# Kernel optimization log

Hardware: AMD Instinct MI355X
Metric: run time of the kernel (lower is better)

## Reference

```python
import jax, jax.numpy as jnp
import numpy as np

TEMPERATURE = 11.313708498984761  # sqrt(d_k) with d_k=128
RELU15_CAP = 15.0


def setup_inputs() -> dict:
    key = jax.random.key(0)
    kq, kk, kv = jax.random.split(key, 3)
    B, H, S, D = 4, 16, 1024, 128
    q = jax.random.normal(kq, (B, H, S, D), dtype=jnp.float32)
    k = jax.random.normal(kk, (B, H, S, D), dtype=jnp.float32)
    v = jax.random.normal(kv, (B, H, S, D), dtype=jnp.float32)
    mask = jnp.ones((B, 1, S, S), dtype=jnp.int32)  # broadcast over heads
    return {"q": q, "k": k, "v": v, "mask": mask}


def reference(q, k, v, mask):
    # attn = (q / temperature) @ k^T  -> [B,H,Sq,Sk]
    attn = jnp.einsum("bhqd,bhkd->bhqk", q / TEMPERATURE, k)
    # masked_fill(mask == 0, -1e9)
    attn = jnp.where(mask == 0, jnp.float32(-1e9), attn)
    # ReLU15 activation (custom softmax replacement): clamp to [0, 15]
    attn = jnp.clip(attn, 0.0, RELU15_CAP)
    # dropout with p=0.0 is identity (inference reference)
    out = jnp.einsum("bhqk,bhkd->bhqd", attn, v)
    return (out, attn)
```

## Files before the change

kernel.cpp:

```cpp
#include <hip/hip_runtime.h>
#include <stdint.h>

#define B_   4
#define H_   16
#define S_   1024
#define D_   128
#define BM   64
#define BN   32
#define NKT  (S_ / BN)
#define NTHREADS 256

typedef float f32x4 __attribute__((ext_vector_type(4)));
typedef short s16x8 __attribute__((ext_vector_type(8)));
typedef short s16x4 __attribute__((ext_vector_type(4)));

static __device__ __forceinline__ uint16_t f2bf(float f) {
  uint32_t u = __float_as_uint(f);
  u += 0x7FFFu + ((u >> 16) & 1u);
  return (uint16_t)(u >> 16);
}
static __device__ __forceinline__ float bf2f(uint16_t h) {
  return __uint_as_float((uint32_t)h << 16);
}

#define LDS_BARRIER() do {                                   \
    asm volatile("s_waitcnt lgkmcnt(0)" ::: "memory");       \
    __builtin_amdgcn_s_barrier();                            \
    __builtin_amdgcn_sched_barrier(0);                       \
  } while (0)


__global__ __launch_bounds__(NTHREADS)
__attribute__((amdgpu_waves_per_eu(4, 4)))
void attn_relu15_kernel(const float* __restrict__ q, const float* __restrict__ k,
                        const float* __restrict__ v, const int* __restrict__ mask,
                        float* __restrict__ outp, float* __restrict__ attnp)
{
  const int blk = blockIdx.x;
  const int g   = (blk & 7) * 128 + (blk >> 3);
  const int bh  = g >> 4;
  const int qt  = g & 15;
  const int b   = bh >> 4;

  const int tid  = threadIdx.x;
  const int lane = tid & 63;
  const int wq   = tid >> 6;
  const int lhi  = lane >> 4;
  const int llo  = lane & 15;

  __shared__ __align__(16) char smem[36864];
  char* const lK0 = smem;
  char* const lV0 = smem + 16384;
  char* const lS  = smem + 32768 + wq * 1024;

  const float* qg = q + (size_t)bh * (S_ * D_) + (size_t)qt * BM * D_;
  const float* kg = k + (size_t)bh * (S_ * D_);
  const float* vg = v + (size_t)bh * (S_ * D_);
  const int*   mg = mask  + (size_t)b * S_ * S_ + (size_t)qt * BM * S_;
  float*       ag = attnp + (size_t)bh * S_ * S_ + (size_t)qt * BM * S_;
  float*       og = outp  + (size_t)bh * (S_ * D_) + (size_t)qt * BM * D_;

  const float invT = 0.08838834764831843f;

  #define K_O(rep)   ((tid + NTHREADS * (rep)) * 8)
  #define K_ROW(o)   ((((o) >> 10) & 1) * 16 + (((o) >> 4) & 15))
  #define K_COL(o)   (((o) >> 11) * 32 + (((o) >> 8) & 3) * 8 + (((o) >> 3) & 1) * 4)

  s16x8 qf[4];
  {
    const float* qrow = qg + (size_t)(16 * wq + llo) * D_;
    #pragma unroll
    for (int ks = 0; ks < 4; ++ks) {
      int d0 = 32 * ks + 8 * lhi;
      f32x4 x0 = *(const f32x4*)(qrow + d0);
      f32x4 x1 = *(const f32x4*)(qrow + d0 + 4);
      s16x8 h;
      h[0]=f2bf(x0[0]*invT); h[1]=f2bf(x0[1]*invT); h[2]=f2bf(x0[2]*invT); h[3]=f2bf(x0[3]*invT);
      h[4]=f2bf(x1[0]*invT); h[5]=f2bf(x1[1]*invT); h[6]=f2bf(x1[2]*invT); h[7]=f2bf(x1[3]*invT);
      qf[ks] = h;
    }
  }

  {
    #pragma unroll
    for (int rep = 0; rep < 4; ++rep) {
      int o = K_O(rep);
      f32x4 x = *(const f32x4*)(kg + K_ROW(o) * D_ + K_COL(o));
      s16x4 h; h[0]=f2bf(x[0]); h[1]=f2bf(x[1]); h[2]=f2bf(x[2]); h[3]=f2bf(x[3]);
      *(s16x4*)(lK0 + o) = h;
    }
    #pragma unroll
    for (int rep = 0; rep < 4; ++rep) {
      int bid = (tid >> 2) + 64 * rep;
      int kb = bid >> 5, db = bid & 31, l2 = lane & 3;
      f32x4 x = *(const f32x4*)(vg + (size_t)(kb * 4 + l2) * D_ + db * 4);
      float v0=x[0], v1=x[1], v2=x[2], v3=x[3], t;
      t=(l2&1)?v0:v1; t=__shfl_xor(t,1); if(l2&1)v0=t; else v1=t;
      t=(l2&1)?v2:v3; t=__shfl_xor(t,1); if(l2&1)v2=t; else v3=t;
      t=(l2&2)?v0:v2; t=__shfl_xor(t,2); if(l2&2)v0=t; else v2=t;
      t=(l2&2)?v1:v3; t=__shfl_xor(t,2); if(l2&2)v1=t; else v3=t;
      int dd = db * 4 + l2;
      s16x4 h; h[0]=f2bf(v0); h[1]=f2bf(v1); h[2]=f2bf(v2); h[3]=f2bf(v3);
      *(s16x4*)(lV0 + (dd >> 4) * 1024 + ((kb >> 1) & 3) * 256
                    + (dd & 15) * 16 + (kb & 1) * 8) = h;
    }
  }
  LDS_BARRIER();

  f32x4 oacc[8];
  #pragma unroll
  for (int i = 0; i < 8; ++i) oacc[i] = (f32x4){0.f,0.f,0.f,0.f};

  int cur = 0;
  for (int kt = 0; kt < NKT; ++kt) {
    const bool pf = (kt + 1 < NKT);
    char* lKc = lK0 + cur * 8192;
    char* lVc = lV0 + cur * 8192;

    f32x4 kst[4];
    const float* kgt = kg + (size_t)(kt + 1) * BN * D_;
    if (pf) {
      #pragma unroll
      for (int rep = 0; rep < 4; ++rep) {
        int o = K_O(rep);
        kst[rep] = *(const f32x4*)(kgt + K_ROW(o) * D_ + K_COL(o));
      }
    }
    int mreg[8];
    #pragma unroll
    for (int nt = 0; nt < 2; ++nt)
      #pragma unroll
      for (int j = 0; j < 4; ++j)
        mreg[nt * 4 + j] =
          mg[(size_t)(16 * wq + 4 * lhi + j) * S_ + kt * BN + 16 * nt + llo];

    f32x4 sacc[2];
    sacc[0] = (f32x4){0.f,0.f,0.f,0.f}; sacc[1] = sacc[0];
    #pragma unroll
    for (int ks = 0; ks < 4; ++ks) {
      s16x8 bfr[2];
      #pragma unroll
      for (int nt = 0; nt < 2; ++nt)
        bfr[nt] = *(s16x8*)(lKc + (ks * 2 + nt) * 1024 + lane * 16);
      #pragma unroll
      for (int nt = 0; nt < 2; ++nt)
        sacc[nt] = __builtin_amdgcn_mfma_f32_16x16x32_bf16(qf[ks], bfr[nt], sacc[nt], 0, 0, 0);
    }

    f32x4 vst[4];
    const float* vgt = vg + (size_t)(kt + 1) * BN * D_;
    if (pf) {
      char* lKn = lK0 + (cur ^ 1) * 8192;
      #pragma unroll
      for (int rep = 0; rep < 4; ++rep) {
        f32x4 x = kst[rep];
        s16x4 h; h[0]=f2bf(x[0]); h[1]=f2bf(x[1]); h[2]=f2bf(x[2]); h[3]=f2bf(x[3]);
        *(s16x4*)(lKn + K_O(rep)) = h;
      }
      #pragma unroll
      for (int rep = 0; rep < 4; ++rep) {
        int bid = (tid >> 2) + 64 * rep;
        int kb = bid >> 5, db = bid & 31, l2 = lane & 3;
        vst[rep] = *(const f32x4*)(vgt + (size_t)(kb * 4 + l2) * D_ + db * 4);
      }
    }

    #pragma unroll
    for (int nt = 0; nt < 2; ++nt) {
      char* sb = lS + (2 * nt + (llo >> 3)) * 256 + (llo & 7) * 2;
      #pragma unroll
      for (int j = 0; j < 4; ++j) {
        float val = fminf(fmaxf(sacc[nt][j], 0.f), 15.f);
        if (mreg[nt * 4 + j] == 0) val = 0.f;
        *(uint16_t*)(sb + (4 * lhi + j) * 16) = f2bf(val);
      }
    }

    {
      s16x8 saf = *(s16x8*)(lS + lane * 16);
      #pragma unroll
      for (int nt = 0; nt < 8; ++nt) {
        s16x8 vb = *(s16x8*)(lVc + nt * 1024 + lane * 16);
        oacc[nt] = __builtin_amdgcn_mfma_f32_16x16x32_bf16(saf, vb, oacc[nt], 0, 0, 0);
      }
    }

    #pragma unroll
    for (int p = 0; p < 2; ++p) {
      int r  = 16 * wq + p * 8 + (lane >> 3);
      int cb = lane & 7;
      s16x4 sv = *(s16x4*)(lS + (cb >> 1) * 256 + ((r & 15) * 16) + (cb & 1) * 8);
      f32x4 a;
      a[0]=bf2f((uint16_t)sv[0]); a[1]=bf2f((uint16_t)sv[1]);
      a[2]=bf2f((uint16_t)sv[2]); a[3]=bf2f((uint16_t)sv[3]);
      __builtin_nontemporal_store(a, (f32x4*)(ag + (size_t)r * S_ + kt * BN + cb * 4));
    }

    if (pf) {
      char* lVn = lV0 + (cur ^ 1) * 8192;
      #pragma unroll
      for (int rep = 0; rep < 4; ++rep) {
        int bid = (tid >> 2) + 64 * rep;
        int kb = bid >> 5, db = bid & 31, l2 = lane & 3;
        f32x4 x = vst[rep];
        float v0=x[0], v1=x[1], v2=x[2], v3=x[3], t;
        t=(l2&1)?v0:v1; t=__shfl_xor(t,1); if(l2&1)v0=t; else v1=t;
        t=(l2&1)?v2:v3; t=__shfl_xor(t,1); if(l2&1)v2=t; else v3=t;
        t=(l2&2)?v0:v2; t=__shfl_xor(t,2); if(l2&2)v0=t; else v2=t;
        t=(l2&2)?v1:v3; t=__shfl_xor(t,2); if(l2&2)v1=t; else v3=t;
        int dd = db * 4 + l2;
        s16x4 h; h[0]=f2bf(v0); h[1]=f2bf(v1); h[2]=f2bf(v2); h[3]=f2bf(v3);
        *(s16x4*)(lVn + (dd >> 4) * 1024 + ((kb >> 1) & 3) * 256
                      + (dd & 15) * 16 + (kb & 1) * 8) = h;
      }
    }

    LDS_BARRIER();
    cur ^= 1;
  }

  #pragma unroll
  for (int nt = 0; nt < 8; ++nt) {
    int n = 16 * nt + llo;
    #pragma unroll
    for (int j = 0; j < 4; ++j) {
      int m = 16 * wq + 4 * lhi + j;
      __builtin_nontemporal_store(oacc[nt][j], og + (size_t)m * D_ + n);
    }
  }
}

extern "C" void kernel_launch(void* const* d_in, const int* in_sizes, int n_in,
                              void* d_out, int out_size, void* d_ws, size_t ws_size,
                              hipStream_t stream) {
  const float* q    = (const float*)d_in[0];
  const float* k    = (const float*)d_in[1];
  const float* v    = (const float*)d_in[2];
  const int*   mask = (const int*)d_in[3];
  float* outp  = (float*)d_out;
  float* attnp = outp + (size_t)B_ * H_ * S_ * D_;
  dim3 grid(B_ * H_ * (S_ / BM));
  attn_relu15_kernel<<<grid, NTHREADS, 0, stream>>>(q, k, v, mask, outp, attnp);
}
```

Baseline: 125.9 us.

## Pre-convert K/V to bf16 MFMA layout and bitpack mask in a prepass kernel

Adds a prepass kernel that converts K and V to bf16 in the exact LDS fragment layout and packs the int32 mask into bitmasks in workspace. The main kernel then streams K/V tiles straight into LDS with global_load_lds and reads one mask bit per element instead of int32 loads. This removes the repeated per-query-tile fp32 conversion, the shuffle-based transpose and the 4-byte mask reads, at the cost of an extra launch and extra workspace traffic. The original kernel is kept as a fallback when the workspace is too small.

Result: faster. 101.5 us (-19.4%).

```diff
diff --git a/kernel.cpp b/kernel.cpp
--- a/kernel.cpp
+++ b/kernel.cpp
@@ -23,18 +23,63 @@
   return __uint_as_float((uint32_t)h << 16);
 }
 
-#define LDS_BARRIER() do {                                   \
-    asm volatile("s_waitcnt lgkmcnt(0)" ::: "memory");       \
-    __builtin_amdgcn_s_barrier();                            \
-    __builtin_amdgcn_sched_barrier(0);                       \
-  } while (0)
-
+static __device__ __forceinline__ void gl16(const void* g, void* l) {
+  __builtin_amdgcn_global_load_lds(
+      (const __attribute__((address_space(1))) unsigned int*)g,
+      (__attribute__((address_space(3))) unsigned int*)l, 16, 0, 0);
+}
+
+#define WSK_BYTES  16777216
+#define WSV_BYTES  16777216
+#define WSM_BYTES  524288
+#define WS_NEED    (WSK_BYTES + WSV_BYTES + WSM_BYTES)
+
+__global__ __launch_bounds__(256)
+void prepass_kernel(const float* __restrict__ k, const float* __restrict__ v,
+                    const int* __restrict__ mask,
+                    char* __restrict__ wsK, char* __restrict__ wsV,
+                    uint32_t* __restrict__ wsM)
+{
+  int gid = blockIdx.x * 256 + threadIdx.x;
+  if (gid < 1048576) {
+    int tile = gid >> 9, c = gid & 511;
+    int ks = c >> 7, nt = (c >> 6) & 1, lane = c & 63;
+    int row = (tile & 31) * 32 + 16 * nt + (lane & 15);
+    int col = 32 * ks + 8 * (lane >> 4);
+    const float* src = k + ((size_t)(tile >> 5) * S_ + row) * D_ + col;
+    f32x4 x0 = *(const f32x4*)src;
+    f32x4 x1 = *(const f32x4*)(src + 4);
+    s16x8 h;
+    h[0]=f2bf(x0[0]); h[1]=f2bf(x0[1]); h[2]=f2bf(x0[2]); h[3]=f2bf(x0[3]);
+    h[4]=f2bf(x1[0]); h[5]=f2bf(x1[1]); h[6]=f2bf(x1[2]); h[7]=f2bf(x1[3]);
+    *(s16x8*)(wsK + (size_t)gid * 16) = h;
+  } else if (gid < 2097152) {
+    int gv = gid - 1048576;
+    int tile = gv >> 9, c = gv & 511;
+    int nt = c >> 6, lane = c & 63;
+    int d   = 16 * nt + (lane & 15);
+    int kv0 = (tile & 31) * 32 + 8 * (lane >> 4);
+    const float* src = v + ((size_t)(tile >> 5) * S_ + kv0) * D_ + d;
+    s16x8 h;
+    #pragma unroll
+    for (int i = 0; i < 8; ++i) h[i] = f2bf(src[(size_t)i * D_]);
+    *(s16x8*)(wsV + (size_t)gv * 16) = h;
+  } else if (gid < 2228224) {
+    int gm = gid - 2097152;
+    const int* src = mask + (size_t)(gm >> 5) * S_ + (gm & 31) * 32;
+    uint32_t bits = 0;
+    #pragma unroll
+    for (int i = 0; i < 32; ++i) bits |= (src[i] != 0 ? 1u : 0u) << i;
+    wsM[gm] = bits;
+  }
+}
 
 __global__ __launch_bounds__(NTHREADS)
 __attribute__((amdgpu_waves_per_eu(4, 4)))
-void attn_relu15_kernel(const float* __restrict__ q, const float* __restrict__ k,
-                        const float* __restrict__ v, const int* __restrict__ mask,
-                        float* __restrict__ outp, float* __restrict__ attnp)
+void attn_relu15_main(const float* __restrict__ q,
+                      const char* __restrict__ wsK, const char* __restrict__ wsV,
+                      const uint32_t* __restrict__ wsM,
+                      float* __restrict__ outp, float* __restrict__ attnp)
 {
   const int blk = blockIdx.x;
   const int g   = (blk & 7) * 128 + (blk >> 3);
@@ -53,18 +98,14 @@
   char* const lV0 = smem + 16384;
   char* const lS  = smem + 32768 + wq * 1024;
 
-  const float* qg = q + (size_t)bh * (S_ * D_) + (size_t)qt * BM * D_;
-  const float* kg = k + (size_t)bh * (S_ * D_);
-  const float* vg = v + (size_t)bh * (S_ * D_);
-  const int*   mg = mask  + (size_t)b * S_ * S_ + (size_t)qt * BM * S_;
-  float*       ag = attnp + (size_t)bh * S_ * S_ + (size_t)qt * BM * S_;
-  float*       og = outp  + (size_t)bh * (S_ * D_) + (size_t)qt * BM * D_;
+  const float*    qg = q + (size_t)bh * (S_ * D_) + (size_t)qt * BM * D_;
+  const char*     kw = wsK + (size_t)(bh * 32) * 8192;
+  const char*     vw = wsV + (size_t)(bh * 32) * 8192;
+  const uint32_t* mw0 = wsM + ((size_t)b * S_ + qt * BM + 16 * wq) * 32;
+  float*          ag = attnp + (size_t)bh * S_ * S_ + (size_t)qt * BM * S_;
+  float*          og = outp  + (size_t)bh * (S_ * D_) + (size_t)qt * BM * D_;
 
   const float invT = 0.08838834764831843f;
-
-  #define K_O(rep)   ((tid + NTHREADS * (rep)) * 8)
-  #define K_ROW(o)   ((((o) >> 10) & 1) * 16 + (((o) >> 4) & 15))
-  #define K_COL(o)   (((o) >> 11) * 32 + (((o) >> 8) & 3) * 8 + (((o) >> 3) & 1) * 4)
 
   s16x8 qf[4];
   {
@@ -81,6 +122,158 @@
     }
   }
 
+  #pragma unroll
+  for (int rep = 0; rep < 2; ++rep) {
+    gl16(kw + rep * 4096 + tid * 16, lK0 + rep * 4096 + wq * 1024);
+    gl16(vw + rep * 4096 + tid * 16, lV0 + rep * 4096 + wq * 1024);
+  }
+  asm volatile("s_waitcnt vmcnt(0) lgkmcnt(0)" ::: "memory");
+  __builtin_amdgcn_s_barrier();
+  __builtin_amdgcn_sched_barrier(0);
+
+  f32x4 oacc[8];
+  #pragma unroll
+  for (int i = 0; i < 8; ++i) oacc[i] = (f32x4){0.f,0.f,0.f,0.f};
+
+  int cur = 0;
+  for (int kt = 0; kt < NKT; ++kt) {
+    const bool pf = (kt + 1 < NKT);
+    char* lKc = lK0 + cur * 8192;
+    char* lVc = lV0 + cur * 8192;
+
+    uint32_t mwv[4];
+    #pragma unroll
+    for (int j = 0; j < 4; ++j)
+      mwv[j] = mw0[(size_t)(4 * lhi + j) * 32 + kt];
+
+    if (pf) {
+      const char* kn = kw + (size_t)(kt + 1) * 8192;
+      const char* vn = vw + (size_t)(kt + 1) * 8192;
+      char* lKn = lK0 + (cur ^ 1) * 8192;
+      char* lVn = lV0 + (cur ^ 1) * 8192;
+      #pragma unroll
+      for (int rep = 0; rep < 2; ++rep) {
+        gl16(kn + rep * 4096 + tid * 16, lKn + rep * 4096 + wq * 1024);
+        gl16(vn + rep * 4096 + tid * 16, lVn + rep * 4096 + wq * 1024);
+      }
+    }
+    __builtin_amdgcn_sched_barrier(0);
+
+    f32x4 sacc[2];
+    sacc[0] = (f32x4){0.f,0.f,0.f,0.f}; sacc[1] = sacc[0];
+    #pragma unroll
+    for (int ks = 0; ks < 4; ++ks) {
+      s16x8 bfr[2];
+      #pragma unroll
+      for (int nt = 0; nt < 2; ++nt)
+        bfr[nt] = *(s16x8*)(lKc + (ks * 2 + nt) * 1024 + lane * 16);
+      #pragma unroll
+      for (int nt = 0; nt < 2; ++nt)
+        sacc[nt] = __builtin_amdgcn_mfma_f32_16x16x32_bf16(qf[ks], bfr[nt], sacc[nt], 0, 0, 0);
+    }
+
+    #pragma unroll
+    for (int nt = 0; nt < 2; ++nt) {
+      char* sb = lS + (2 * nt + (llo >> 3)) * 256 + (llo & 7) * 2;
+      #pragma unroll
+      for (int j = 0; j < 4; ++j) {
+        float val = fminf(fmaxf(sacc[nt][j], 0.f), 15.f);
+        if (!((mwv[j] >> (16 * nt + llo)) & 1u)) val = 0.f;
+        *(uint16_t*)(sb + (4 * lhi + j) * 16) = f2bf(val);
+      }
+    }
+
+    #pragma unroll
+    for (int p = 0; p < 2; ++p) {
+      int r  = 16 * wq + p * 8 + (lane >> 3);
+      int cb = lane & 7;
+      s16x4 sv = *(s16x4*)(lS + (cb >> 1) * 256 + ((r & 15) * 16) + (cb & 1) * 8);
+      f32x4 a;
+      a[0]=bf2f((uint16_t)sv[0]); a[1]=bf2f((uint16_t)sv[1]);
+      a[2]=bf2f((uint16_t)sv[2]); a[3]=bf2f((uint16_t)sv[3]);
+      __builtin_nontemporal_store(a, (f32x4*)(ag + (size_t)r * S_ + kt * BN + cb * 4));
+    }
+
+    {
+      s16x8 saf = *(s16x8*)(lS + lane * 16);
+      #pragma unroll
+      for (int nt = 0; nt < 8; ++nt) {
+        s16x8 vb = *(s16x8*)(lVc + nt * 1024 + lane * 16);
+        oacc[nt] = __builtin_amdgcn_mfma_f32_16x16x32_bf16(saf, vb, oacc[nt], 0, 0, 0);
+      }
+    }
+
+    asm volatile("s_waitcnt vmcnt(2) lgkmcnt(0)" ::: "memory");
+    __builtin_amdgcn_s_barrier();
+    __builtin_amdgcn_sched_barrier(0);
+    cur ^= 1;
+  }
+
+  #pragma unroll
+  for (int nt = 0; nt < 8; ++nt) {
+    int n = 16 * nt + llo;
+    #pragma unroll
+    for (int j = 0; j < 4; ++j) {
+      int m = 16 * wq + 4 * lhi + j;
+      __builtin_nontemporal_store(oacc[nt][j], og + (size_t)m * D_ + n);
+    }
+  }
+}
+
+#define LDS_BARRIER() do {                                   \
+    asm volatile("s_waitcnt lgkmcnt(0)" ::: "memory");       \
+    __builtin_amdgcn_s_barrier();                            \
+    __builtin_amdgcn_sched_barrier(0);                       \
+  } while (0)
+
+__global__ __launch_bounds__(NTHREADS)
+__attribute__((amdgpu_waves_per_eu(4, 4)))
+void attn_relu15_fallback(const float* __restrict__ q, const float* __restrict__ k,
+                          const float* __restrict__ v, const int* __restrict__ mask,
+                          float* __restrict__ outp, float* __restrict__ attnp)
+{
+  const int blk = blockIdx.x;
+  const int g   = (blk & 7) * 128 + (blk >> 3);
+  const int bh  = g >> 4;
+  const int qt  = g & 15;
+  const int b   = bh >> 4;
+  const int tid  = threadIdx.x;
+  const int lane = tid & 63;
+  const int wq   = tid >> 6;
+  const int lhi  = lane >> 4;
+  const int llo  = lane & 15;
+
+  __shared__ __align__(16) char smem[36864];
+  char* const lK0 = smem;
+  char* const lV0 = smem + 16384;
+  char* const lS  = smem + 32768 + wq * 1024;
+
+  const float* qg = q + (size_t)bh * (S_ * D_) + (size_t)qt * BM * D_;
+  const float* kg = k + (size_t)bh * (S_ * D_);
+  const float* vg = v + (size_t)bh * (S_ * D_);
+  const int*   mg = mask  + (size_t)b * S_ * S_ + (size_t)qt * BM * S_;
+  float*       ag = attnp + (size_t)bh * S_ * S_ + (size_t)qt * BM * S_;
+  float*       og = outp  + (size_t)bh * (S_ * D_) + (size_t)qt * BM * D_;
+  const float invT = 0.08838834764831843f;
+
+  #define K_O(rep)   ((tid + NTHREADS * (rep)) * 8)
+  #define K_ROW(o)   ((((o) >> 10) & 1) * 16 + (((o) >> 4) & 15))
+  #define K_COL(o)   (((o) >> 11) * 32 + (((o) >> 8) & 3) * 8 + (((o) >> 3) & 1) * 4)
+
+  s16x8 qf[4];
+  {
+    const float* qrow = qg + (size_t)(16 * wq + llo) * D_;
+    #pragma unroll
+    for (int ks = 0; ks < 4; ++ks) {
+      int d0 = 32 * ks + 8 * lhi;
+      f32x4 x0 = *(const f32x4*)(qrow + d0);
+      f32x4 x1 = *(const f32x4*)(qrow + d0 + 4);
+      s16x8 h;
+      h[0]=f2bf(x0[0]*invT); h[1]=f2bf(x0[1]*invT); h[2]=f2bf(x0[2]*invT); h[3]=f2bf(x0[3]*invT);
+      h[4]=f2bf(x1[0]*invT); h[5]=f2bf(x1[1]*invT); h[6]=f2bf(x1[2]*invT); h[7]=f2bf(x1[3]*invT);
+      qf[ks] = h;
+    }
+  }
   {
     #pragma unroll
     for (int rep = 0; rep < 4; ++rep) {
@@ -116,7 +309,6 @@
     const bool pf = (kt + 1 < NKT);
     char* lKc = lK0 + cur * 8192;
     char* lVc = lV0 + cur * 8192;
-
     f32x4 kst[4];
     const float* kgt = kg + (size_t)(kt + 1) * BN * D_;
     if (pf) {
@@ -175,7 +367,6 @@
         *(uint16_t*)(sb + (4 * lhi + j) * 16) = f2bf(val);
       }
     }
-
     {
       s16x8 saf = *(s16x8*)(lS + lane * 16);
       #pragma unroll
@@ -184,7 +375,6 @@
         oacc[nt] = __builtin_amdgcn_mfma_f32_16x16x32_bf16(saf, vb, oacc[nt], 0, 0, 0);
       }
     }
-
     #pragma unroll
     for (int p = 0; p < 2; ++p) {
       int r  = 16 * wq + p * 8 + (lane >> 3);
@@ -195,7 +385,6 @@
       a[2]=bf2f((uint16_t)sv[2]); a[3]=bf2f((uint16_t)sv[3]);
       __builtin_nontemporal_store(a, (f32x4*)(ag + (size_t)r * S_ + kt * BN + cb * 4));
     }
-
     if (pf) {
       char* lVn = lV0 + (cur ^ 1) * 8192;
       #pragma unroll
@@ -214,11 +403,9 @@
                       + (dd & 15) * 16 + (kb & 1) * 8) = h;
       }
     }
-
     LDS_BARRIER();
     cur ^= 1;
   }
-
   #pragma unroll
   for (int nt = 0; nt < 8; ++nt) {
     int n = 16 * nt + llo;
@@ -239,6 +426,16 @@
   const int*   mask = (const int*)d_in[3];
   float* outp  = (float*)d_out;
   float* attnp = outp + (size_t)B_ * H_ * S_ * D_;
-  dim3 grid(B_ * H_ * (S_ / BM));
-  attn_relu15_kernel<<<grid, NTHREADS, 0, stream>>>(q, k, v, mask, outp, attnp);
-}
+
+  if (ws_size >= (size_t)WS_NEED && d_ws != nullptr) {
+    char*     wsK = (char*)d_ws;
+    char*     wsV = wsK + WSK_BYTES;
+    uint32_t* wsM = (uint32_t*)(wsK + WSK_BYTES + WSV_BYTES);
+    prepass_kernel<<<8704, 256, 0, stream>>>(k, v, mask, wsK, wsV, wsM);
+    attn_relu15_main<<<dim3(B_ * H_ * (S_ / BM)), NTHREADS, 0, stream>>>(
+        q, wsK, wsV, wsM, outp, attnp);
+  } else {
+    attn_relu15_fallback<<<dim3(B_ * H_ * (S_ / BM)), NTHREADS, 0, stream>>>(
+        q, k, v, mask, outp, attnp);
+  }
+}
```
